# Kernel tuning notes

Hardware: AMD Instinct MI355X
Metric: run time of the kernel (lower is better)

Reference implementation:

```python
import jax, jax.numpy as jnp
import numpy as np

B, T, C = 32, 512, 1024
H, D = 16, 64
BLOCK_SIZE = 512


def setup_inputs() -> dict:
    key = jax.random.key(0)
    ks = jax.random.split(key, 6)
    s_in = 1.0 / np.sqrt(C)
    return {
        "x": jax.random.normal(ks[0], (B, T, C), dtype=jnp.float32),
        "wq": jax.random.normal(ks[1], (H, C, D), dtype=jnp.float32) * s_in,
        "wk": jax.random.normal(ks[2], (H, C, D), dtype=jnp.float32) * s_in,
        "wv": jax.random.normal(ks[3], (H, C, D), dtype=jnp.float32) * s_in,
        "w_proj": jax.random.normal(ks[4], (C, C), dtype=jnp.float32) * s_in,
        "b_proj": jax.random.normal(ks[5], (C,), dtype=jnp.float32) * 0.01,
    }


def reference(x, wq, wk, wv, w_proj, b_proj):
    b, t, c = x.shape
    # per-head projections (bias=False Linears stacked on head axis)
    q = jnp.einsum("btc,hcd->bhtd", x, wq)
    k = jnp.einsum("btc,hcd->bhtd", x, wk)
    v = jnp.einsum("btc,hcd->bhtd", x, wv)
    # NOTE: original scales by 1/sqrt(C) with C = n_embd, not head_size
    scale = 1.0 / (c ** 0.5)
    scores = jnp.einsum("bhtd,bhsd->bhts", q, k) * scale  # [B,H,T,T]
    causal = jnp.tril(jnp.ones((t, t), dtype=bool))
    scores = jnp.where(causal, scores, jnp.finfo(scores.dtype).min)
    attn = jax.nn.softmax(scores, axis=-1)
    out = jnp.einsum("bhts,bhsd->bhtd", attn, v)
    # concat heads in order -> [B,T,H*D]
    out = out.transpose(0, 2, 1, 3).reshape(b, t, -1)
    # output projection (dropout = identity in eval mode)
    return out @ w_proj + b_proj
```

## Files before the change

kernel.cpp:

```cpp
#include <hip/hip_runtime.h>

typedef unsigned int u32;
typedef unsigned short u16;
typedef __bf16 bf16x8 __attribute__((ext_vector_type(8)));
typedef float f32x4 __attribute__((ext_vector_type(4)));
typedef u16 u16x8 __attribute__((ext_vector_type(8)));
typedef u16 u16x4 __attribute__((ext_vector_type(4)));

#define DEVI static __device__ __forceinline__

DEVI u16 f2bf(float f) {
  union { float f; u32 u; } v; v.f = f;
  return (u16)((v.u + 0x7fffu + ((v.u >> 16) & 1u)) >> 16);
}

DEVI u32 cvtpk(float a, float b) {
  u32 r;
  asm("v_cvt_pk_bf16_f32 %0, %1, %2" : "=v"(r) : "v"(a), "v"(b));
  return r;
}

constexpr long QS_ = 16777216;
constexpr long XB_O    = 0;
constexpr long WQKV_O  = 16777216;
constexpr long Q_O     = 19922944;
constexpr long CTX_O   = 70254592;
constexpr long WPROJ_O = 87031808;

__global__ __launch_bounds__(256) void k_cast_x(const float* __restrict__ x, u16* __restrict__ xb) {
  long i = (long)blockIdx.x * 256 + threadIdx.x;
  const float4* p = (const float4*)(x + i * 8);
  float4 a = p[0], b = p[1];
  u16x8 r;
  r[0]=f2bf(a.x); r[1]=f2bf(a.y); r[2]=f2bf(a.z); r[3]=f2bf(a.w);
  r[4]=f2bf(b.x); r[5]=f2bf(b.y); r[6]=f2bf(b.z); r[7]=f2bf(b.w);
  *(u16x8*)(xb + i * 8) = r;
}

__global__ __launch_bounds__(256) void k_prep_wqkv(const float* __restrict__ wq, const float* __restrict__ wk,
                                                   const float* __restrict__ wv, u16* __restrict__ wt) {
  long o = (long)blockIdx.x * 256 + threadIdx.x;
  int n = (int)(o >> 10), kk = (int)(o & 1023);
  int sel = n >> 10, h = (n >> 6) & 15, d = n & 63;
  const float* W = (sel == 0) ? wq : ((sel == 1) ? wk : wv);
  wt[o] = f2bf(W[((long)h * 1024 + kk) * 64 + d]);
}

__global__ __launch_bounds__(256) void k_prep_wproj(const float* __restrict__ wp, u16* __restrict__ wt) {
  long o = (long)blockIdx.x * 256 + threadIdx.x;
  int n = (int)(o >> 10), kk = (int)(o & 1023);
  wt[o] = f2bf(wp[(long)kk * 1024 + n]);
}

DEVI void gload16(const u16* g, u16* l) {
  __builtin_amdgcn_global_load_lds((const __attribute__((address_space(1))) u32*)g,
                                   (__attribute__((address_space(3))) u32*)l, 16, 0, 0);
}

template <int NN, int EPI>
__global__ __launch_bounds__(512, 2)
void k_gemm(const u16* __restrict__ A, const u16* __restrict__ Bt,
            u16* __restrict__ oq, float* __restrict__ of, const float* __restrict__ bias) {
  __shared__ u16 lds[2][4][8192];

  const int tid = threadIdx.x;
  const int lane = tid & 63;
  const int w = tid >> 6;
  const int wm = w >> 2, wn = w & 3;
  const int lg = lane >> 4, lr = lane & 15;
  const int bht = 2 + (wn >> 1);
  const int bn0 = (wn & 1) * 4;

  constexpr int NBN = NN / 256;
  const int nwg = gridDim.x;
  const int swz = ((int)blockIdx.x & 7) * (nwg >> 3) + ((int)blockIdx.x >> 3);
  const long m0 = (long)(swz / NBN) * 256, n0 = (long)(swz % NBN) * 256;

  int srcoff[2];
  #pragma unroll
  for (int r2 = 0; r2 < 2; ++r2) {
    int s = r2 * 8 + w;
    int mi = s >> 1, ks = s & 1;
    int rowl = mi * 16 + (lane >> 2);
    int colu = ks * 32 + (((lane & 3) * 8) ^ (((lane >> 5) & 1) * 16));
    srcoff[r2] = rowl * 1024 + colu;
  }
  const int fo = lr * 32 + ((lg * 8) ^ (((lr >> 3) & 1) * 16));

  const u16* At  = A  + m0 * 1024;
  const u16* Bt2 = Bt + n0 * 1024;

  f32x4 acc[8][4] = {};
  bf16x8 af[4][2];
  bf16x8 bf[4][2];

#define STAGE(buf_, ht_, gbase_)                                               \
  { _Pragma("unroll") for (int r_ = 0; r_ < 2; ++r_)                           \
      gload16((gbase_) + srcoff[r_], &lds[buf_][ht_][r_ * 4096 + w * 512]); }

#define LDS_A(buf_, milo_)                                                     \
  { _Pragma("unroll") for (int i_ = 0; i_ < 4; ++i_)                           \
    _Pragma("unroll") for (int ks_ = 0; ks_ < 2; ++ks_)                        \
      af[i_][ks_] = *(const bf16x8*)&lds[buf_][wm][((milo_ + i_) * 2 + ks_) * 512 + fo]; }

#define LDS_B(buf_, nilo_)                                                     \
  { _Pragma("unroll") for (int j_ = 0; j_ < 2; ++j_)                           \
    _Pragma("unroll") for (int ks_ = 0; ks_ < 2; ++ks_)                        \
      bf[nilo_ + j_][ks_] = *(const bf16x8*)&lds[buf_][bht][((bn0 + nilo_ + j_) * 2 + ks_) * 512 + fo]; }

#define QUAD(milo_, nilo_)                                                     \
  { __builtin_amdgcn_s_setprio(1);                                             \
    _Pragma("unroll") for (int ks_ = 0; ks_ < 2; ++ks_)                        \
    _Pragma("unroll") for (int i_ = 0; i_ < 4; ++i_)                           \
    _Pragma("unroll") for (int j_ = 0; j_ < 2; ++j_)                           \
      acc[milo_ + i_][nilo_ + j_] = __builtin_amdgcn_mfma_f32_16x16x32_bf16(   \
          af[i_][ks_], bf[nilo_ + j_][ks_], acc[milo_ + i_][nilo_ + j_], 0, 0, 0); \
    __builtin_amdgcn_s_setprio(0); }

#define WAIT_LGKM() { asm volatile("s_waitcnt lgkmcnt(0)" ::: "memory");       \
                      __builtin_amdgcn_sched_barrier(0); }

  STAGE(0, 0, At);
  STAGE(0, 1, At + 131072);
  STAGE(0, 2, Bt2);
  STAGE(0, 3, Bt2 + 131072);
  STAGE(1, 0, At + 64);
  STAGE(1, 1, At + 131072 + 64);
  STAGE(1, 2, Bt2 + 64);
  STAGE(1, 3, Bt2 + 131072 + 64);
  asm volatile("s_waitcnt vmcnt(8)" ::: "memory");
  __builtin_amdgcn_s_barrier();

  #pragma unroll 1
  for (int t = 0; t < 16; ++t) {
    const int buf = t & 1;
    LDS_A(buf, 0); LDS_B(buf, 0);
    __builtin_amdgcn_s_barrier();
    WAIT_LGKM();
    QUAD(0, 0);
    __builtin_amdgcn_s_barrier();
    LDS_B(buf, 2);
    __builtin_amdgcn_s_barrier();
    WAIT_LGKM();
    QUAD(0, 2);
    __builtin_amdgcn_s_barrier();
    LDS_A(buf, 4);
    if (t + 2 < 16) {
      STAGE(buf, 2, Bt2 + (t + 2) * 64);
      STAGE(buf, 3, Bt2 + 131072 + (t + 2) * 64);
    }
    __builtin_amdgcn_s_barrier();
    WAIT_LGKM();
    QUAD(4, 2);
    __builtin_amdgcn_s_barrier();
    if (t + 2 < 16) {
      STAGE(buf, 0, At + (t + 2) * 64);
      STAGE(buf, 1, At + 131072 + (t + 2) * 64);
    }
    __builtin_amdgcn_s_barrier();
    QUAD(4, 0);
    if (t < 14)       { asm volatile("s_waitcnt vmcnt(8)" ::: "memory"); }
    else if (t == 14) { asm volatile("s_waitcnt vmcnt(0)" ::: "memory"); }
    __builtin_amdgcn_s_barrier();
  }

  if constexpr (EPI == 0) {
    #pragma unroll
    for (int mi = 0; mi < 8; ++mi) {
      int grow = (int)m0 + wm * 128 + mi * 16 + lg * 4;
      int b = grow >> 9, t0 = grow & 511;
      #pragma unroll
      for (int ni = 0; ni < 4; ++ni) {
        int gcol = (int)n0 + wn * 64 + ni * 16 + lr;
        int sel = gcol >> 10, h = (gcol >> 6) & 15, d = gcol & 63;
        u16* dst = oq + (long)sel * QS_ + (((long)(b * 16 + h) * 512 + t0) * 64 + d);
        #pragma unroll
        for (int r = 0; r < 4; ++r) dst[r * 64] = f2bf(acc[mi][ni][r]);
      }
    }
  } else {
    float bv[4];
    #pragma unroll
    for (int ni = 0; ni < 4; ++ni) bv[ni] = bias[(int)n0 + wn * 64 + ni * 16 + lr];
    #pragma unroll
    for (int mi = 0; mi < 8; ++mi) {
      int grow = (int)m0 + wm * 128 + mi * 16 + lg * 4;
      #pragma unroll
      for (int ni = 0; ni < 4; ++ni) {
        int gcol = (int)n0 + wn * 64 + ni * 16 + lr;
        #pragma unroll
        for (int r = 0; r < 4; ++r)
          of[(long)(grow + r) * NN + gcol] = acc[mi][ni][r] + bv[ni];
      }
    }
  }
#undef STAGE
#undef LDS_A
#undef LDS_B
#undef QUAD
#undef WAIT_LGKM
}

__global__ __launch_bounds__(256, 3)
void k_attn(const u16* __restrict__ Qp, const u16* __restrict__ Kp,
            const u16* __restrict__ Vp, u16* __restrict__ ctx) {
  __shared__ u16 k_lds[2][64 * 72];
  __shared__ u16 vt_lds[2][64 * 72];

  const int bid = blockIdx.x;
  const int qi = 3 - (bid >> 9);
  const int bh = bid & 511;
  const int tid = threadIdx.x, lane = tid & 63, w = tid >> 6;
  const int lg = lane >> 4, lr = lane & 15;
  const long base = (long)bh * (512 * 64);

  const int q0 = qi * 128 + w * 32;

  bf16x8 qf[2][2];
  #pragma unroll
  for (int mt = 0; mt < 2; ++mt)
    #pragma unroll
    for (int k2 = 0; k2 < 2; ++k2)
      qf[mt][k2] = *(const bf16x8*)(Qp + base + (long)(q0 + mt * 16 + lr) * 64 + k2 * 32 + lg * 8);

  f32x4 o[2][4] = {};
  float ms[2] = {-1e30f, -1e30f};
  float ls[2] = {0.f, 0.f};

  const int nch = (qi + 1) * 2;
  int srow[2], scol[2], cslot[2];
  #pragma unroll
  for (int i = 0; i < 2; ++i) {
    int s = i * 256 + tid;
    srow[i] = s >> 3; scol[i] = s & 7;
    int sr = srow[i];
    cslot[i] = ((sr >> 5) << 5) + (((sr >> 2) & 3) << 3) + (((sr >> 4) & 1) << 2) + (sr & 3);
  }

  uint4 kreg[2], vreg[2];
  auto loadch = [&](int c) {
    #pragma unroll
    for (int i = 0; i < 2; ++i) {
      long go = base + (long)(c * 64 + srow[i]) * 64 + scol[i] * 8;
      kreg[i] = *(const uint4*)(Kp + go);
      vreg[i] = *(const uint4*)(Vp + go);
    }
  };
  auto writech = [&](int bsel) {
    #pragma unroll
    for (int i = 0; i < 2; ++i) {
      *(uint4*)&k_lds[bsel][srow[i] * 72 + scol[i] * 8] = kreg[i];
      union { uint4 v; u16 s[8]; } t; t.v = vreg[i];
      #pragma unroll
      for (int j = 0; j < 8; ++j)
        vt_lds[bsel][(scol[i] * 8 + j) * 72 + cslot[i]] = t.s[j];
    }
  };

  loadch(0);
  writech(0);
  loadch(1);
  __syncthreads();

  const float sc = 0.045084220027780106f;

  #pragma unroll 1
  for (int c = 0; c < nch; ++c) {
    const int bsel = c & 1;
    if (c + 1 < nch) writech(bsel ^ 1);
    if (c + 2 < nch) loadch(c + 2);

    if (c * 64 <= q0 + 31) {
      const bool full = (c * 64 + 63 <= q0);
      f32x4 st[2][4] = {};
      bf16x8 kf2[4][2];
      #pragma unroll
      for (int nt = 0; nt < 4; ++nt)
        #pragma unroll
        for (int k2 = 0; k2 < 2; ++k2)
          kf2[nt][k2] = *(const bf16x8*)&k_lds[bsel][(nt * 16 + lr) * 72 + k2 * 32 + lg * 8];
      __builtin_amdgcn_s_setprio(1);
      #pragma unroll
      for (int k2 = 0; k2 < 2; ++k2)
        #pragma unroll
        for (int mt = 0; mt < 2; ++mt)
          #pragma unroll
          for (int nt = 0; nt < 4; ++nt)
            st[mt][nt] = __builtin_amdgcn_mfma_f32_16x16x32_bf16(kf2[nt][k2], qf[mt][k2], st[mt][nt], 0, 0, 0);
      __builtin_amdgcn_s_setprio(0);

      u32 pkw[2][4][2];
      #pragma unroll
      for (int mt = 0; mt < 2; ++mt) {
        const int q = q0 + mt * 16 + lr;
        if (!full) {
          #pragma unroll
          for (int nt = 0; nt < 4; ++nt)
            #pragma unroll
            for (int r = 0; r < 4; ++r) {
              int s_ = c * 64 + nt * 16 + lg * 4 + r;
              st[mt][nt][r] = (s_ <= q) ? st[mt][nt][r] : -1e30f;
            }
        }
        float mx = st[mt][0][0];
        #pragma unroll
        for (int nt = 0; nt < 4; ++nt)
          #pragma unroll
          for (int r = 0; r < 4; ++r) mx = fmaxf(mx, st[mt][nt][r]);
        mx = fmaxf(mx, __shfl_xor(mx, 16));
        mx = fmaxf(mx, __shfl_xor(mx, 32));
        const float mnew = fmaxf(ms[mt], mx);
        const float alpha = exp2f((ms[mt] - mnew) * sc);
        ms[mt] = mnew;
        const float msc = mnew * sc;
        float ps = 0.f;
        float p[4][4];
        #pragma unroll
        for (int nt = 0; nt < 4; ++nt)
          #pragma unroll
          for (int r = 0; r < 4; ++r) {
            float pv = exp2f(fmaf(st[mt][nt][r], sc, -msc));
            p[nt][r] = pv;
            ps += pv;
          }
        ps += __shfl_xor(ps, 16);
        ps += __shfl_xor(ps, 32);
        ls[mt] = ls[mt] * alpha + ps;
        #pragma unroll
        for (int nt = 0; nt < 4; ++nt) {
          pkw[mt][nt][0] = cvtpk(p[nt][0], p[nt][1]);
          pkw[mt][nt][1] = cvtpk(p[nt][2], p[nt][3]);
        }
        #pragma unroll
        for (int dt = 0; dt < 4; ++dt) o[mt][dt] *= alpha;
      }

      bf16x8 vf2[4][2];
      #pragma unroll
      for (int dt = 0; dt < 4; ++dt)
        #pragma unroll
        for (int k2 = 0; k2 < 2; ++k2)
          vf2[dt][k2] = *(const bf16x8*)&vt_lds[bsel][(dt * 16 + lr) * 72 + k2 * 32 + lg * 8];
      __builtin_amdgcn_s_setprio(1);
      #pragma unroll
      for (int k2 = 0; k2 < 2; ++k2)
        #pragma unroll
        for (int mt = 0; mt < 2; ++mt) {
          union { u32 w4[4]; bf16x8 v; } pb;
          pb.w4[0] = pkw[mt][2 * k2][0];
          pb.w4[1] = pkw[mt][2 * k2][1];
          pb.w4[2] = pkw[mt][2 * k2 + 1][0];
          pb.w4[3] = pkw[mt][2 * k2 + 1][1];
          #pragma unroll
          for (int dt = 0; dt < 4; ++dt)
            o[mt][dt] = __builtin_amdgcn_mfma_f32_16x16x32_bf16(vf2[dt][k2], pb.v, o[mt][dt], 0, 0, 0);
        }
      __builtin_amdgcn_s_setprio(0);
    }
    __syncthreads();
  }

  const int b = bh >> 4, h = bh & 15;
  #pragma unroll
  for (int mt = 0; mt < 2; ++mt) {
    const int t = q0 + mt * 16 + lr;
    const float inv = 1.0f / ls[mt];
    #pragma unroll
    for (int dt = 0; dt < 4; ++dt) {
      u16x4 pk4;
      #pragma unroll
      for (int r = 0; r < 4; ++r) pk4[r] = f2bf(o[mt][dt][r] * inv);
      *(u16x4*)(ctx + ((long)(b * 512 + t)) * 1024 + h * 64 + dt * 16 + lg * 4) = pk4;
    }
  }
}

extern "C" void kernel_launch(void* const* d_in, const int* in_sizes, int n_in,
                              void* d_out, int out_size, void* d_ws, size_t ws_size,
                              hipStream_t stream) {
  const float* x  = (const float*)d_in[0];
  const float* wq = (const float*)d_in[1];
  const float* wk = (const float*)d_in[2];
  const float* wv = (const float*)d_in[3];
  const float* wp = (const float*)d_in[4];
  const float* bp = (const float*)d_in[5];
  float* out = (float*)d_out;
  u16* ws = (u16*)d_ws;

  u16* XB    = ws + XB_O;
  u16* WQKV  = ws + WQKV_O;
  u16* Qb    = ws + Q_O;
  u16* CTX   = ws + CTX_O;
  u16* WPROJ = ws + WPROJ_O;

  k_cast_x<<<8192, 256, 0, stream>>>(x, XB);
  k_prep_wqkv<<<12288, 256, 0, stream>>>(wq, wk, wv, WQKV);
  k_prep_wproj<<<4096, 256, 0, stream>>>(wp, WPROJ);
  k_gemm<3072, 0><<<(16384 / 256) * (3072 / 256), 512, 0, stream>>>(XB, WQKV, Qb, nullptr, nullptr);
  k_attn<<<2048, 256, 0, stream>>>(Qb, Qb + QS_, Qb + 2 * QS_, CTX);
  k_gemm<1024, 1><<<(16384 / 256) * (1024 / 256), 512, 0, stream>>>(CTX, WPROJ, nullptr, out, bp);
}
```

Measured before the change: 253.0 us.

## Software-pipeline LDS fragment loads with MFMA in GEMM main loop

```diff
diff --git a/kernel.cpp b/kernel.cpp
--- a/kernel.cpp
+++ b/kernel.cpp
@@ -91,34 +91,33 @@
   const u16* Bt2 = Bt + n0 * 1024;
 
   f32x4 acc[8][4] = {};
-  bf16x8 af[4][2];
-  bf16x8 bf[4][2];
+  bf16x8 aq[2][2][2];
+  bf16x8 bfr[4][2];
 
 #define STAGE(buf_, ht_, gbase_)                                               \
   { _Pragma("unroll") for (int r_ = 0; r_ < 2; ++r_)                           \
       gload16((gbase_) + srcoff[r_], &lds[buf_][ht_][r_ * 4096 + w * 512]); }
 
-#define LDS_A(buf_, milo_)                                                     \
-  { _Pragma("unroll") for (int i_ = 0; i_ < 4; ++i_)                           \
+#define LDS_AQ(set_, buf_, q_)                                                 \
+  { _Pragma("unroll") for (int i_ = 0; i_ < 2; ++i_)                           \
     _Pragma("unroll") for (int ks_ = 0; ks_ < 2; ++ks_)                        \
-      af[i_][ks_] = *(const bf16x8*)&lds[buf_][wm][((milo_ + i_) * 2 + ks_) * 512 + fo]; }
-
-#define LDS_B(buf_, nilo_)                                                     \
+      aq[set_][i_][ks_] = *(const bf16x8*)&lds[buf_][wm][(((q_)*2 + i_) * 2 + ks_) * 512 + fo]; }
+
+#define LDS_BF(buf_, lo_)                                                      \
   { _Pragma("unroll") for (int j_ = 0; j_ < 2; ++j_)                           \
     _Pragma("unroll") for (int ks_ = 0; ks_ < 2; ++ks_)                        \
-      bf[nilo_ + j_][ks_] = *(const bf16x8*)&lds[buf_][bht][((bn0 + nilo_ + j_) * 2 + ks_) * 512 + fo]; }
-
-#define QUAD(milo_, nilo_)                                                     \
+      bfr[(lo_) + j_][ks_] = *(const bf16x8*)&lds[buf_][bht][((bn0 + (lo_) + j_) * 2 + ks_) * 512 + fo]; }
+
+#define QUAD8(set_, q_, lo_)                                                   \
   { __builtin_amdgcn_s_setprio(1);                                             \
     _Pragma("unroll") for (int ks_ = 0; ks_ < 2; ++ks_)                        \
-    _Pragma("unroll") for (int i_ = 0; i_ < 4; ++i_)                           \
+    _Pragma("unroll") for (int i_ = 0; i_ < 2; ++i_)                           \
     _Pragma("unroll") for (int j_ = 0; j_ < 2; ++j_)                           \
-      acc[milo_ + i_][nilo_ + j_] = __builtin_amdgcn_mfma_f32_16x16x32_bf16(   \
-          af[i_][ks_], bf[nilo_ + j_][ks_], acc[milo_ + i_][nilo_ + j_], 0, 0, 0); \
+      acc[(q_)*2 + i_][(lo_) + j_] = __builtin_amdgcn_mfma_f32_16x16x32_bf16(  \
+          aq[set_][i_][ks_], bfr[(lo_) + j_][ks_], acc[(q_)*2 + i_][(lo_) + j_], 0, 0, 0); \
     __builtin_amdgcn_s_setprio(0); }
 
-#define WAIT_LGKM() { asm volatile("s_waitcnt lgkmcnt(0)" ::: "memory");       \
-                      __builtin_amdgcn_sched_barrier(0); }
+#define BARF() { asm volatile("s_barrier" ::: "memory"); }
 
   STAGE(0, 0, At);
   STAGE(0, 1, At + 131072);
@@ -129,39 +128,44 @@
   STAGE(1, 2, Bt2 + 64);
   STAGE(1, 3, Bt2 + 131072 + 64);
   asm volatile("s_waitcnt vmcnt(8)" ::: "memory");
-  __builtin_amdgcn_s_barrier();
+  BARF();
+  LDS_AQ(0, 0, 0);
+  LDS_BF(0, 0);
 
   #pragma unroll 1
   for (int t = 0; t < 16; ++t) {
     const int buf = t & 1;
-    LDS_A(buf, 0); LDS_B(buf, 0);
-    __builtin_amdgcn_s_barrier();
-    WAIT_LGKM();
-    QUAD(0, 0);
-    __builtin_amdgcn_s_barrier();
-    LDS_B(buf, 2);
-    __builtin_amdgcn_s_barrier();
-    WAIT_LGKM();
-    QUAD(0, 2);
-    __builtin_amdgcn_s_barrier();
-    LDS_A(buf, 4);
-    if (t + 2 < 16) {
-      STAGE(buf, 2, Bt2 + (t + 2) * 64);
-      STAGE(buf, 3, Bt2 + 131072 + (t + 2) * 64);
-    }
-    __builtin_amdgcn_s_barrier();
-    WAIT_LGKM();
-    QUAD(4, 2);
-    __builtin_amdgcn_s_barrier();
-    if (t + 2 < 16) {
-      STAGE(buf, 0, At + (t + 2) * 64);
-      STAGE(buf, 1, At + 131072 + (t + 2) * 64);
-    }
-    __builtin_amdgcn_s_barrier();
-    QUAD(4, 0);
+    LDS_BF(buf, 2);
+    LDS_AQ(1, buf, 1);
+    QUAD8(0, 0, 0);
+    BARF();
+    QUAD8(0, 0, 2);
+    BARF();
+    LDS_AQ(0, buf, 2);
+    if (t + 2 < 16) { STAGE(buf, 2, Bt2 + (t + 2) * 64); STAGE(buf, 3, Bt2 + 131072 + (t + 2) * 64); }
+    QUAD8(1, 1, 0);
+    BARF();
+    QUAD8(1, 1, 2);
+    BARF();
+    LDS_AQ(1, buf, 3);
+    QUAD8(0, 2, 0);
+    BARF();
+    QUAD8(0, 2, 2);
+    asm volatile("s_waitcnt lgkmcnt(0)" ::: "memory");
+    __builtin_amdgcn_sched_barrier(0);
+    BARF();
+    if (t + 2 < 16) { STAGE(buf, 0, At + (t + 2) * 64); STAGE(buf, 1, At + 131072 + (t + 2) * 64); }
+    QUAD8(1, 3, 0);
+    BARF();
     if (t < 14)       { asm volatile("s_waitcnt vmcnt(8)" ::: "memory"); }
     else if (t == 14) { asm volatile("s_waitcnt vmcnt(0)" ::: "memory"); }
-    __builtin_amdgcn_s_barrier();
+    BARF();
+    if (t + 1 < 16) {
+      LDS_AQ(0, buf ^ 1, 0);
+      LDS_BF(buf ^ 1, 0);
+    }
+    QUAD8(1, 3, 2);
+    BARF();
   }
 
   if constexpr (EPI == 0) {
@@ -195,10 +199,10 @@
     }
   }
 #undef STAGE
-#undef LDS_A
-#undef LDS_B
-#undef QUAD
-#undef WAIT_LGKM
+#undef LDS_AQ
+#undef LDS_BF
+#undef QUAD8
+#undef BARF
 }
 
 __global__ __launch_bounds__(256, 3)
```

After: 250.7 us. Within noise of the previous version (-0.9%).
